# Kernel optimization log

Hardware: AMD Instinct MI355X
Metric: run time of the kernel (lower is better)

Reference implementation:

```python
import jax, jax.numpy as jnp
import numpy as np

K = 7          # kernel_size
DIL = 1        # dilation
TOPK = 8       # top_k
EPS = 1e-8     # torch cosine_similarity eps
W_SRC_POS = W_SRC_NEG = W_SIM_POS = W_SIM_NEG = 1.0


def unfold(x):
    # x: [B, C, H, W] -> [B, C, K*K, H, W]  (torch nn.Unfold ordering: c, kh, kw)
    B, C, H, W = x.shape
    pad = (K // 2) * DIL
    xp = jnp.pad(x, ((0, 0), (0, 0), (pad, pad), (pad, pad)))
    pats = [xp[:, :, i * DIL:i * DIL + H, j * DIL:j * DIL + W]
            for i in range(K) for j in range(K)]
    return jnp.stack(pats, axis=2)


def cosine_sim_feat(x):
    # local cosine similarity between each pixel and its KxK neighborhood
    unf = unfold(x)                                    # [B,C,K2,H,W]
    dot = jnp.einsum('bckhw,bchw->bkhw', unf, x)       # [B,K2,H,W]
    n_u = jnp.sqrt(jnp.sum(unf * unf, axis=1))         # [B,K2,H,W]
    n_x = jnp.sqrt(jnp.sum(x * x, axis=1))             # [B,H,W]
    return dot / (jnp.maximum(n_u, EPS) * jnp.maximum(n_x[:, None], EPS))


def masked_mean(x, mask):
    m = jnp.broadcast_to(mask, x.shape).astype(x.dtype)
    return jnp.sum(x * m) / jnp.maximum(jnp.sum(m), 1.0)


def reference(logits_trg, gt_src, x_ema, x_src, mix_masks, img_trg):
    # ---- masks ----
    ign_src = gt_src != 255                              # [B,1,H,W] bool
    ign_trg = (1.0 - mix_masks) > 0.5                    # [B,1,H,W] bool

    # ---- source pos/neg local cosine similarity ----
    sim_src = cosine_sim_feat(x_src)                     # [B,K2,H,W]
    unf_gt = unfold(gt_src.astype(jnp.float32))[:, 0].astype(jnp.int32)  # [B,K2,H,W]
    pos_pair = unf_gt == gt_src[:, 0][:, None]           # [B,K2,H,W]
    neg_pair = ~pos_pair
    src_pos = masked_mean(sim_src, pos_pair & ign_src)
    src_neg = masked_mean(sim_src, neg_pair & ign_src)

    # ---- target: cross class-agreement prob with neighbors ----
    sim_ema = cosine_sim_feat(x_ema)                     # [B,K2,H,W]
    p = jax.nn.softmax(logits_trg, axis=1)               # [B,C,H,W]
    unf_p = jax.nn.softmax(unfold(logits_trg), axis=1)   # [B,C,K2,H,W]
    cross_pos = jnp.einsum('bchw,bckhw->bkhw', p, unf_p) # [B,K2,H,W]

    # ---- top-k select over the K2 neighborhood axis ----
    s = jnp.moveaxis(sim_ema, 1, -1)                     # [B,H,W,K2]
    cp = jnp.moveaxis(cross_pos, 1, -1)                  # [B,H,W,K2]
    max_v, max_i = jax.lax.top_k(s, TOPK + 1)            # most-similar neighbors
    nmin_v, min_i = jax.lax.top_k(-s, TOPK)              # least-similar neighbors
    min_v = -nmin_v
    cpos_g = jnp.take_along_axis(cp, max_i, axis=-1)
    cneg_g = jnp.take_along_axis(1.0 - cp, min_i, axis=-1)
    loc_pos = max_v * -cpos_g
    loc_neg = (1.0 - min_v) * -cneg_g

    m_trg = jnp.moveaxis(ign_trg, 1, -1)                 # [B,H,W,1]
    loss_sim_pos = masked_mean(loc_pos, m_trg)
    loss_sim_neg = masked_mean(loc_neg, m_trg)

    return jnp.stack([-src_pos * W_SRC_POS,
                      src_neg * W_SRC_NEG,
                      loss_sim_pos * W_SIM_POS,
                      loss_sim_neg * W_SIM_NEG])


def setup_inputs() -> dict:
    key = jax.random.key(0)
    k1, k2, k3, k4, k5, k6 = jax.random.split(key, 6)
    B, C, H, W = 2, 19, 128, 128
    CH = 64
    return {
        'logits_trg': jax.random.normal(k1, (B, C, H, W), dtype=jnp.float32),
        'gt_src': jax.random.randint(k2, (B, 1, H, W), 0, C, dtype=jnp.int32),
        'x_ema': jax.random.normal(k3, (B, CH, H, W), dtype=jnp.float32),
        'x_src': jax.random.normal(k4, (B, CH, H, W), dtype=jnp.float32),
        'mix_masks': jax.random.randint(k5, (B, 1, H, W), 0, 2).astype(jnp.float32),
        'img_trg': jax.random.normal(k6, (B, 3, H, W), dtype=jnp.float32),
    }
```

## Files before the change

### kernel.cpp

```cpp
#include <hip/hip_runtime.h>
#include <math.h>

typedef unsigned short u16;
typedef unsigned int   u32;
typedef unsigned long long u64;

#define Cc   19
#define HWs  16384
#define NPIX 32768
#define FSTR 64
#define PSTR 24
#define NV   196
#define NTILE 512
#define UNIF19 0x2ABD2ABDu

typedef _Float16 h2    __attribute__((ext_vector_type(2)));
typedef _Float16 half8 __attribute__((ext_vector_type(8)));
typedef float  floatx4 __attribute__((ext_vector_type(4)));

__device__ inline float fd(u32 a, u32 b, float c) {
  h2 ha = __builtin_bit_cast(h2, a);
  h2 hb = __builtin_bit_cast(h2, b);
#if __has_builtin(__builtin_amdgcn_fdot2)
  return __builtin_amdgcn_fdot2(ha, hb, c, false);
#else
  return c + (float)ha[0] * (float)hb[0] + (float)ha[1] * (float)hb[1];
#endif
}

__device__ inline u32 pk(float a, float b) {
  h2 h; h[0] = (_Float16)a; h[1] = (_Float16)b;
  return __builtin_bit_cast(u32, h);
}

__global__ __launch_bounds__(256) void pre_kernel(
    const float* __restrict__ logits,
    const float* __restrict__ xsrc, const float* __restrict__ xema,
    u16* __restrict__ osrc, u16* __restrict__ oema, u16* __restrict__ pt) {
  __shared__ float smem[5376];
  int bid = blockIdx.x;
  int t = threadIdx.x;

  if (bid < 1024) {
    float* tile = smem;
    float* part = smem + 4160;
    float* invn = smem + 4416;
    int xb = bid & 255, b = (bid >> 8) & 1, z = bid >> 9;
    const float* in = z ? xema : xsrc;
    u16* out = z ? oema : osrc;
    int pix0 = xb * 64;
    int w = t >> 6, l = t & 63;

    const float* src = in + (size_t)b * 64 * HWs + pix0;
#pragma unroll
    for (int cc = 0; cc < 16; cc++) {
      int c = cc * 4 + w;
      tile[c * 65 + l] = src[(size_t)c * HWs + l];
    }
    __syncthreads();
    float s = 0.f;
#pragma unroll
    for (int c = w * 16; c < w * 16 + 16; c++) { float a = tile[c * 65 + l]; s += a * a; }
    part[w * 64 + l] = s;
    __syncthreads();
    if (t < 64) {
      float n = part[t] + part[64 + t] + part[128 + t] + part[192 + t];
      invn[t] = rsqrtf(fmaxf(n, 1e-16f));
    }
    __syncthreads();
    for (int i = t; i < 512; i += 256) {
      int px = i >> 3, q = i & 7;
      float iv = invn[px];
      float v[8];
#pragma unroll
      for (int k = 0; k < 8; k++) v[k] = tile[(q * 8 + k) * 65 + px] * iv;
      uint4 u = make_uint4(pk(v[0], v[1]), pk(v[2], v[3]), pk(v[4], v[5]), pk(v[6], v[7]));
      *((uint4*)(out + (size_t)(b * HWs + pix0 + px) * FSTR) + q) = u;
    }
  } else {
    float* lp = smem;
    int pb = bid - 1024;
    int gpix = pb * 256 + t;
    int b = gpix >> 14, hw = gpix & (HWs - 1);
    const float* lg = logits + (size_t)b * Cc * HWs + hw;
    float s = 0.f;
    float v[Cc];
#pragma unroll
    for (int c = 0; c < Cc; c++) { v[c] = __expf(lg[(size_t)c * HWs]); s += v[c]; }
    float inv = 1.0f / s;
#pragma unroll
    for (int c = 0; c < Cc; c++) lp[t * 21 + c] = v[c] * inv;
    __syncthreads();
    u16* ob = pt + (size_t)pb * 256 * PSTR;
    for (int i = t; i < 768; i += 256) {
      int px = i / 3, q = i - px * 3;
      float v8[8];
#pragma unroll
      for (int k = 0; k < 8; k++) {
        int c = q * 8 + k;
        v8[k] = (c < Cc) ? lp[px * 21 + c] : 0.f;
      }
      uint4 u = make_uint4(pk(v8[0], v8[1]), pk(v8[2], v8[3]), pk(v8[4], v8[5]), pk(v8[6], v8[7]));
      *((uint4*)(ob + (size_t)px * PSTR) + q) = u;
    }
  }
}

__global__ __launch_bounds__(512, 4) void st_kernel(
    const u16* __restrict__ fsrc, const u16* __restrict__ fema,
    const u16* __restrict__ pt, const int* __restrict__ gt,
    const float* __restrict__ mix, float* __restrict__ partials) {
  __shared__ uint4 fsb[1568];
  __shared__ uint4 feb[1568];
  __shared__ uint4 prb[588];
  __shared__ _Float16 Csc[4][16][113];
  __shared__ int   gtt[NV];
  __shared__ float mixs[64];
  __shared__ u32   ksh[8][64];
  __shared__ float sacc[8][8];

  int bid = blockIdx.x;
  int swz = ((bid & 7) << 6) | (bid >> 3);
  int t = threadIdx.x, wv = t >> 6, lane = t & 63;
  int b  = swz >> 8;
  int th = (swz >> 4) & 15, tw = swz & 15;
  int h0 = th << 3, w0 = tw << 3;

  int nr = lane / 7, nc = lane - nr * 7;
  bool lact = lane < 49;

  const uint4* FS = (const uint4*)fsrc;
  const uint4* FE = (const uint4*)fema;
  for (int i = t; i < 3136; i += 512) {
    int ii = (i >= 1568) ? (i - 1568) : i;
    int vec = ii >> 3, q = ii & 7;
    int r = vec / 14, c = vec - r * 14;
    int gh = h0 + r - 3, gw = w0 + c - 3;
    uint4 d = make_uint4(0u, 0u, 0u, 0u);
    if (((unsigned)gh < 128u) && ((unsigned)gw < 128u)) {
      size_t gidx = ((size_t)((b << 14) | (gh << 7) | gw) << 3) + q;
      d = (i >= 1568) ? FE[gidx] : FS[gidx];
    }
    (i >= 1568 ? feb : fsb)[(vec << 3) | (q ^ (vec & 7))] = d;
  }
  const uint4* PT3 = (const uint4*)pt;
  for (int i = t; i < 588; i += 512) {
    int vec = i / 3, q = i - vec * 3;
    int r = vec / 14, c = vec - r * 14;
    int gh = h0 + r - 3, gw = w0 + c - 3;
    uint4 d = make_uint4(UNIF19, UNIF19, UNIF19, UNIF19);
    if (((unsigned)gh < 128u) && ((unsigned)gw < 128u))
      d = PT3[(size_t)((b << 14) | (gh << 7) | gw) * 3 + q];
    prb[vec * 3 + q] = d;
  }
  for (int i = t; i < NV; i += 512) {
    int r = i / 14, c = i - r * 14;
    int gh = h0 + r - 3, gw = w0 + c - 3;
    int g = 0;
    if (((unsigned)gh < 128u) && ((unsigned)gw < 128u))
      g = gt[(b << 14) | (gh << 7) | gw];
    gtt[i] = g;
  }
  if (t < 64) {
    int r = t >> 3, c = t & 7;
    mixs[t] = mix[(b << 14) | ((h0 + r) << 7) | (w0 + c)];
  }
  __syncthreads();

  int rt = wv >> 1, hf = wv & 1;
  int p16 = lane & 15, gq = lane >> 4;
  int va = (2 * rt + (p16 >> 3) + 3) * 14 + ((p16 & 7) + 3);
  int ntiles = hf ? 3 : 4;
  int cb0 = hf ? 64 : 0;
  int vb0 = 28 * rt + cb0;

  {
    half8 a0 = __builtin_bit_cast(half8, fsb[(va << 3) | ((gq    ) ^ (va & 7))]);
    half8 a1 = __builtin_bit_cast(half8, fsb[(va << 3) | ((gq + 4) ^ (va & 7))]);
    for (int ct = 0; ct < ntiles; ct++) {
      int vb = vb0 + ct * 16 + p16;
      half8 b0 = __builtin_bit_cast(half8, fsb[(vb << 3) | ((gq    ) ^ (vb & 7))]);
      half8 b1 = __builtin_bit_cast(half8, fsb[(vb << 3) | ((gq + 4) ^ (vb & 7))]);
      floatx4 a4 = {0.f, 0.f, 0.f, 0.f};
      a4 = __builtin_amdgcn_mfma_f32_16x16x32_f16(a0, b0, a4, 0, 0, 0);
      a4 = __builtin_amdgcn_mfma_f32_16x16x32_f16(a1, b1, a4, 0, 0, 0);
      int row = gq << 2, col = cb0 + ct * 16 + p16;
#pragma unroll
      for (int r = 0; r < 4; r++) Csc[rt][row + r][col] = (_Float16)a4[r];
    }
  }
  __syncthreads();

  float psum = 0, ssum = 0, posa = 0, nega = 0, pcntW = 0, vcntW = 0, cntW = 0;
  int ri = wv & 1;

  for (int tc = 0; tc < 8; ++tc) {
    int vcH = (wv + 3) * 14 + (tc + 3);
    int gtcv = gtt[vcH];
    if (gtcv != 255) {
      int cbi = lact ? ((ri + nr) * 14 + (tc + nc)) : 0;
      float sims = (float)Csc[rt][ri * 8 + tc][cbi];
      int vnH = lact ? ((wv + nr) * 14 + (tc + nc)) : vcH;
      int gtn = gtt[vnH];
      bool pos = (gtn == gtcv);
      if (lact) { ssum += sims; if (pos) psum += sims; }
      u64 mk = __ballot(lact && pos);
      pcntW += (float)__popcll(mk);
      vcntW += 1.f;
    }
  }
  __syncthreads();

  {
    half8 a0 = __builtin_bit_cast(half8, feb[(va << 3) | ((gq    ) ^ (va & 7))]);
    half8 a1 = __builtin_bit_cast(half8, feb[(va << 3) | ((gq + 4) ^ (va & 7))]);
    for (int ct = 0; ct < ntiles; ct++) {
      int vb = vb0 + ct * 16 + p16;
      half8 b0 = __builtin_bit_cast(half8, feb[(vb << 3) | ((gq    ) ^ (vb & 7))]);
      half8 b1 = __builtin_bit_cast(half8, feb[(vb << 3) | ((gq + 4) ^ (vb & 7))]);
      floatx4 a4 = {0.f, 0.f, 0.f, 0.f};
      a4 = __builtin_amdgcn_mfma_f32_16x16x32_f16(a0, b0, a4, 0, 0, 0);
      a4 = __builtin_amdgcn_mfma_f32_16x16x32_f16(a1, b1, a4, 0, 0, 0);
      int row = gq << 2, col = cb0 + ct * 16 + p16;
#pragma unroll
      for (int r = 0; r < 4; r++) Csc[rt][row + r][col] = (_Float16)a4[r];
    }
  }
  __syncthreads();

  for (int tc = 0; tc < 8; ++tc) {
    if (mixs[(wv << 3) | tc] < 0.5f) {
      int vcH = (wv + 3) * 14 + (tc + 3);
      int vnH = lact ? ((wv + nr) * 14 + (tc + nc)) : vcH;
      int cbi = lact ? ((ri + nr) * 14 + (tc + nc)) : 0;
      float v = lact ? (float)Csc[rt][ri * 8 + tc][cbi] : 0.f;

      uint4 pA = prb[vnH * 3 + 0], pB = prb[vnH * 3 + 1], pC = prb[vnH * 3 + 2];
      uint4 qA = prb[vcH * 3 + 0], qB = prb[vcH * 3 + 1], qC = prb[vcH * 3 + 2];
      float p0 = 0, p1 = 0, p2 = 0;
      p0 = fd(qA.x,pA.x,p0); p0 = fd(qA.y,pA.y,p0); p0 = fd(qA.z,pA.z,p0); p0 = fd(qA.w,pA.w,p0);
      p1 = fd(qB.x,pB.x,p1); p1 = fd(qB.y,pB.y,p1); p1 = fd(qB.z,pB.z,p1); p1 = fd(qB.w,pB.w,p1);
      p2 = fd(qC.x,pC.x,p2); p2 = fd(qC.y,pC.y,p2); p2 = fd(qC.z,pC.z,p2); p2 = fd(qC.w,pC.w,p2);
      float cp = (p0 + p1) + p2;

      u32 bits = __float_as_uint(v);
      u32 mono = (bits & 0x80000000u) ? ~bits : (bits | 0x80000000u);
      u32 key = (mono & 0xFFFFFFC0u) | (u32)lane;
      ksh[wv][lane] = key;
      int rd = 0;
      const uint4* kr = (const uint4*)ksh[wv];
#pragma unroll
      for (int j = 0; j < 12; j++) {
        uint4 qq = kr[j];
        rd += (qq.x > key); rd += (qq.y > key); rd += (qq.z > key); rd += (qq.w > key);
      }
      rd += (ksh[wv][48] > key);
      if (lact) {
        if (rd < 9)   posa += v * cp;
        if (rd >= 41) nega += (1.f - v) * (1.f - cp);
      }
      cntW += 1.f;
    }
  }

#pragma unroll
  for (int off = 32; off; off >>= 1) {
    psum += __shfl_xor(psum, off); ssum += __shfl_xor(ssum, off);
    posa += __shfl_xor(posa, off); nega += __shfl_xor(nega, off);
  }
  if (lane == 0) {
    sacc[wv][0] = psum;  sacc[wv][1] = pcntW; sacc[wv][2] = ssum;
    sacc[wv][3] = posa;  sacc[wv][4] = nega;  sacc[wv][5] = vcntW;
    sacc[wv][6] = cntW;  sacc[wv][7] = 0.f;
  }
  __syncthreads();
  if (t < 8) {
    float s = 0.f;
#pragma unroll
    for (int k = 0; k < 8; k++) s += sacc[k][t];
    partials[(size_t)bid * 8 + t] = s;
  }
}

__global__ __launch_bounds__(256) void finish_kernel(
    const float* __restrict__ partials, float* __restrict__ out) {
  int t = threadIdx.x, lane = t & 63, wv = t >> 6;
  float s0=0,s1=0,s2=0,s3=0,s4=0,s5=0,s6=0;
  for (int r = t; r < NTILE; r += 256) {
    const float4* p = (const float4*)(partials + (size_t)r * 8);
    float4 x = p[0], y = p[1];
    s0 += x.x; s1 += x.y; s2 += x.z; s3 += x.w;
    s4 += y.x; s5 += y.y; s6 += y.z;
  }
#pragma unroll
  for (int off = 32; off; off >>= 1) {
    s0 += __shfl_xor(s0, off); s1 += __shfl_xor(s1, off);
    s2 += __shfl_xor(s2, off); s3 += __shfl_xor(s3, off);
    s4 += __shfl_xor(s4, off); s5 += __shfl_xor(s5, off);
    s6 += __shfl_xor(s6, off);
  }
  __shared__ float sacc[4][8];
  if (lane == 0) {
    sacc[wv][0]=s0; sacc[wv][1]=s1; sacc[wv][2]=s2; sacc[wv][3]=s3;
    sacc[wv][4]=s4; sacc[wv][5]=s5; sacc[wv][6]=s6;
  }
  __syncthreads();
  if (t == 0) {
    float a[7];
#pragma unroll
    for (int c = 0; c < 7; c++) a[c] = sacc[0][c] + sacc[1][c] + sacc[2][c] + sacc[3][c];
    float psum = a[0], pcnt = a[1], ssum = a[2];
    float posa = a[3], nega = a[4], vcnt = a[5], cnt = a[6];
    float nsum = ssum - psum;
    float ncnt = 49.f * vcnt - pcnt;
    out[0] = -(psum / fmaxf(pcnt, 1.0f));
    out[1] =  (nsum / fmaxf(ncnt, 1.0f));
    out[2] = -(posa / fmaxf(9.0f * cnt, 1.0f));
    out[3] = -(nega / fmaxf(8.0f * cnt, 1.0f));
  }
}

extern "C" void kernel_launch(void* const* d_in, const int* in_sizes, int n_in,
                              void* d_out, int out_size, void* d_ws, size_t ws_size,
                              hipStream_t stream) {
  const float* logits = (const float*)d_in[0];
  const int*   gt     = (const int*)  d_in[1];
  const float* xema   = (const float*)d_in[2];
  const float* xsrc   = (const float*)d_in[3];
  const float* mix    = (const float*)d_in[4];
  float* out = (float*)d_out;

  float* partials = (float*)d_ws;
  u16* fsrc = (u16*)((char*)d_ws + NTILE * 8 * sizeof(float));
  u16* fema = fsrc + (size_t)NPIX * FSTR;
  u16* pt   = fema + (size_t)NPIX * FSTR;

  pre_kernel<<<1152, 256, 0, stream>>>(logits, xsrc, xema, fsrc, fema, pt);
  st_kernel<<<NTILE, 512, 0, stream>>>(fsrc, fema, pt, gt, mix, partials);
  finish_kernel<<<1, 256, 0, stream>>>(partials, out);
}
```

Baseline: 30.32 us.

## Stage EMA features in registers and reuse source LDS buffer to raise occupancy

Removes the separate 25 KB LDS buffer for EMA features. The EMA tile is instead prefetched into registers at kernel start and written into the source-feature buffer after the source cosine pass has finished. The launch bound goes from 4 to 6 blocks per CU, so more blocks can be resident. The trade-off is higher register pressure from holding four uint4 per thread across the source phase, and a possible cap on occupancy from the 6-block register limit.

```diff
diff --git a/kernel.cpp b/kernel.cpp
--- a/kernel.cpp
+++ b/kernel.cpp
@@ -106,12 +106,11 @@
   }
 }
 
-__global__ __launch_bounds__(512, 4) void st_kernel(
+__global__ __launch_bounds__(512, 6) void st_kernel(
     const u16* __restrict__ fsrc, const u16* __restrict__ fema,
     const u16* __restrict__ pt, const int* __restrict__ gt,
     const float* __restrict__ mix, float* __restrict__ partials) {
   __shared__ uint4 fsb[1568];
-  __shared__ uint4 feb[1568];
   __shared__ uint4 prb[588];
   __shared__ _Float16 Csc[4][16][113];
   __shared__ int   gtt[NV];
@@ -131,17 +130,30 @@
 
   const uint4* FS = (const uint4*)fsrc;
   const uint4* FE = (const uint4*)fema;
-  for (int i = t; i < 3136; i += 512) {
-    int ii = (i >= 1568) ? (i - 1568) : i;
-    int vec = ii >> 3, q = ii & 7;
+
+  uint4 E[4];
+#pragma unroll
+  for (int k = 0; k < 4; k++) {
+    int i = t + k * 512;
+    uint4 d = make_uint4(0u, 0u, 0u, 0u);
+    if (i < 1568) {
+      int vec = i >> 3, q = i & 7;
+      int r = vec / 14, c = vec - r * 14;
+      int gh = h0 + r - 3, gw = w0 + c - 3;
+      if (((unsigned)gh < 128u) && ((unsigned)gw < 128u))
+        d = FE[((size_t)((b << 14) | (gh << 7) | gw) << 3) + q];
+    }
+    E[k] = d;
+  }
+
+  for (int i = t; i < 1568; i += 512) {
+    int vec = i >> 3, q = i & 7;
     int r = vec / 14, c = vec - r * 14;
     int gh = h0 + r - 3, gw = w0 + c - 3;
     uint4 d = make_uint4(0u, 0u, 0u, 0u);
-    if (((unsigned)gh < 128u) && ((unsigned)gw < 128u)) {
-      size_t gidx = ((size_t)((b << 14) | (gh << 7) | gw) << 3) + q;
-      d = (i >= 1568) ? FE[gidx] : FS[gidx];
-    }
-    (i >= 1568 ? feb : fsb)[(vec << 3) | (q ^ (vec & 7))] = d;
+    if (((unsigned)gh < 128u) && ((unsigned)gw < 128u))
+      d = FS[((size_t)((b << 14) | (gh << 7) | gw) << 3) + q];
+    fsb[(vec << 3) | (q ^ (vec & 7))] = d;
   }
   const uint4* PT3 = (const uint4*)pt;
   for (int i = t; i < 588; i += 512) {
@@ -190,6 +202,15 @@
     }
   }
   __syncthreads();
+
+#pragma unroll
+  for (int k = 0; k < 4; k++) {
+    int i = t + k * 512;
+    if (i < 1568) {
+      int vec = i >> 3, q = i & 7;
+      fsb[(vec << 3) | (q ^ (vec & 7))] = E[k];
+    }
+  }
 
   float psum = 0, ssum = 0, posa = 0, nega = 0, pcntW = 0, vcntW = 0, cntW = 0;
   int ri = wv & 1;
@@ -212,12 +233,12 @@
   __syncthreads();
 
   {
-    half8 a0 = __builtin_bit_cast(half8, feb[(va << 3) | ((gq    ) ^ (va & 7))]);
-    half8 a1 = __builtin_bit_cast(half8, feb[(va << 3) | ((gq + 4) ^ (va & 7))]);
+    half8 a0 = __builtin_bit_cast(half8, fsb[(va << 3) | ((gq    ) ^ (va & 7))]);
+    half8 a1 = __builtin_bit_cast(half8, fsb[(va << 3) | ((gq + 4) ^ (va & 7))]);
     for (int ct = 0; ct < ntiles; ct++) {
       int vb = vb0 + ct * 16 + p16;
-      half8 b0 = __builtin_bit_cast(half8, feb[(vb << 3) | ((gq    ) ^ (vb & 7))]);
-      half8 b1 = __builtin_bit_cast(half8, feb[(vb << 3) | ((gq + 4) ^ (vb & 7))]);
+      half8 b0 = __builtin_bit_cast(half8, fsb[(vb << 3) | ((gq    ) ^ (vb & 7))]);
+      half8 b1 = __builtin_bit_cast(half8, fsb[(vb << 3) | ((gq + 4) ^ (vb & 7))]);
       floatx4 a4 = {0.f, 0.f, 0.f, 0.f};
       a4 = __builtin_amdgcn_mfma_f32_16x16x32_f16(a0, b0, a4, 0, 0, 0);
       a4 = __builtin_amdgcn_mfma_f32_16x16x32_f16(a1, b1, a4, 0, 0, 0);
```

Result: no change. 30.28 us (-0.1%).
